# Performance work log

Measured on AMD Instinct MI355X. Metric: run time of the kernel, lower is better.

## Reference

```python
import jax, jax.numpy as jnp
import numpy as np

N_NODES = 50000
N_EDGES = 800000
D_IN = 512
LATENT = [512, 512, 512]
L2_EPS = 1e-12  # torch F.normalize clamp_min


def _gin_layer(x, src, dst, W, b, eps):
    # sum aggregation of neighbor (source) features into destination nodes
    agg = jax.ops.segment_sum(x[src], dst, num_segments=x.shape[0])  # [N, d]
    h = agg + (1.0 + eps) * x
    return jax.nn.relu(h @ W + b)  # Sequential(Linear, ReLU)


def _l2_normalize(x):
    n = jnp.sqrt(jnp.sum(x * x, axis=-1, keepdims=True))
    return x / jnp.maximum(n, L2_EPS)


def setup_inputs() -> dict:
    key = jax.random.key(0)
    ks = jax.random.split(key, 10)
    x = jax.random.normal(ks[0], (N_NODES, D_IN), dtype=jnp.float32)
    edge_index = jax.random.randint(ks[1], (2, N_EDGES), 0, N_NODES, dtype=jnp.int32)
    dims = [D_IN] + LATENT
    inp = {"x": x, "edge_index": edge_index}
    for i in range(3):
        fan_in = dims[i]
        bound = 1.0 / np.sqrt(fan_in)
        inp[f"W{i+1}"] = jax.random.uniform(ks[2 + 2 * i], (dims[i], dims[i + 1]), jnp.float32, -bound, bound)
        inp[f"b{i+1}"] = jax.random.uniform(ks[3 + 2 * i], (dims[i + 1],), jnp.float32, -bound, bound)
        inp[f"eps{i+1}"] = jnp.zeros((), dtype=jnp.float32)  # train_eps=True, init 0
    return inp


def reference(x, edge_index, W1, b1, eps1, W2, b2, eps2, W3, b3, eps3):
    src, dst = edge_index[0], edge_index[1]
    # layers 0..num_layers-2: GINConv -> L2 normalize -> ReLU
    h = _gin_layer(x, src, dst, W1, b1, eps1)
    h = jax.nn.relu(_l2_normalize(h))
    h = _gin_layer(h, src, dst, W2, b2, eps2)
    h = jax.nn.relu(_l2_normalize(h))
    # final layer: raw GINConv output = logits
    logits = _gin_layer(h, src, dst, W3, b3, eps3)
    probs = jax.nn.softmax(logits, axis=-1)
    return (logits, probs)
```

## Files before the change

kernel.cpp:

```cpp
#include <hip/hip_runtime.h>
#include <stdint.h>

#define N_NODES 50000
#define N_EDGES 800000

typedef unsigned int uint32;

__device__ inline float bflo(uint32 u) { return __builtin_bit_cast(float, u << 16); }
__device__ inline float bfhi(uint32 u) { return __builtin_bit_cast(float, u & 0xffff0000u); }
__device__ inline float bf2f(unsigned short h) { return __builtin_bit_cast(float, (uint32)h << 16); }
__device__ inline unsigned short f2bf(float f) {
    uint32 u = __builtin_bit_cast(uint32, f);
    u += 0x7fffu + ((u >> 16) & 1u);
    return (unsigned short)(u >> 16);
}
__device__ inline uint32 pack2(float lo, float hi) {
    return (uint32)f2bf(lo) | ((uint32)f2bf(hi) << 16);
}

__global__ __launch_bounds__(256) void zero_k(int* p, int n) {
    int i = blockIdx.x * 256 + threadIdx.x;
    if (i < n) p[i] = 0;
}

__global__ __launch_bounds__(256) void count_k(const int* __restrict__ ei, int* __restrict__ cnt) {
    int e = blockIdx.x * 256 + threadIdx.x;
    if (e < N_EDGES) atomicAdd(&cnt[ei[N_EDGES + e]], 1);
}

__global__ __launch_bounds__(1024) void scan_k(int* __restrict__ cnt, int* __restrict__ rowptr) {
    __shared__ int sh[1024];
    const int CH = 49;
    int t = threadIdx.x;
    int base = t * CH;
    int s = 0;
    for (int i = 0; i < CH; i++) {
        int idx = base + i;
        if (idx < N_NODES) s += cnt[idx];
    }
    sh[t] = s;
    __syncthreads();
    for (int d = 1; d < 1024; d <<= 1) {
        int v = (t >= d) ? sh[t - d] : 0;
        __syncthreads();
        sh[t] += v;
        __syncthreads();
    }
    int run = sh[t] - s;
    for (int i = 0; i < CH; i++) {
        int idx = base + i;
        if (idx < N_NODES) {
            int v = cnt[idx];
            rowptr[idx] = run;
            cnt[idx] = run;
            run += v;
        }
    }
    if (t == 1023) rowptr[N_NODES] = sh[1023];
}

__global__ __launch_bounds__(256) void fill_k(const int* __restrict__ ei, int* __restrict__ cursor,
                                              int* __restrict__ csr) {
    int e = blockIdx.x * 256 + threadIdx.x;
    if (e < N_EDGES) {
        int d = ei[N_EDGES + e];
        int p = atomicAdd(&cursor[d], 1);
        csr[p] = ei[e];
    }
}

__global__ __launch_bounds__(256) void wprep_k(const float* __restrict__ W,
                                               unsigned short* __restrict__ Whi,
                                               unsigned short* __restrict__ Wlo) {
    int idx = blockIdx.x * 256 + threadIdx.x;
    int k = idx >> 9, n = idx & 511;
    float w = W[idx];
    unsigned short hi = f2bf(w);
    float lo = w - bf2f(hi);
    Whi[n * 512 + k] = hi;
    Wlo[n * 512 + k] = f2bf(lo);
}

__global__ __launch_bounds__(256) void xconv_k(const float* __restrict__ x, uint32* __restrict__ xb) {
    int i = blockIdx.x * 256 + threadIdx.x;
    float2 v = ((const float2*)x)[i];
    xb[i] = pack2(v.x, v.y);
}

__global__ __launch_bounds__(256) void agg_k(const uint32* __restrict__ xin,
                                             const int* __restrict__ rowptr,
                                             const int* __restrict__ csr,
                                             const float* __restrict__ eps,
                                             uint32* __restrict__ hout) {
    int node = blockIdx.x;
    int t = threadIdx.x;
    int beg = rowptr[node], end = rowptr[node + 1];
    const uint32* xc = xin + t;
    float a0 = 0.f, a1 = 0.f;
    int e = beg;
    for (; e + 4 <= end; e += 4) {
        int n0 = csr[e], n1 = csr[e + 1], n2 = csr[e + 2], n3 = csr[e + 3];
        uint32 u0 = xc[n0 * 256], u1 = xc[n1 * 256], u2 = xc[n2 * 256], u3 = xc[n3 * 256];
        a0 += bflo(u0) + bflo(u1) + bflo(u2) + bflo(u3);
        a1 += bfhi(u0) + bfhi(u1) + bfhi(u2) + bfhi(u3);
    }
    for (; e < end; ++e) {
        uint32 u = xc[csr[e] * 256];
        a0 += bflo(u);
        a1 += bfhi(u);
    }
    float ep = 1.0f + eps[0];
    uint32 us = xc[node * 256];
    float h0 = fmaf(ep, bflo(us), a0);
    float h1 = fmaf(ep, bfhi(us), a1);
    hout[node * 256 + t] = pack2(h0, h1);
}

typedef __bf16 bf16x8 __attribute__((ext_vector_type(8)));
typedef float f32x4 __attribute__((ext_vector_type(4)));

template <bool SPLIT, bool F32OUT>
__global__ __launch_bounds__(256) void gemm_k(const unsigned short* __restrict__ A,
                                              const unsigned short* __restrict__ Whi,
                                              const unsigned short* __restrict__ Wlo,
                                              const float* __restrict__ bias,
                                              unsigned short* __restrict__ outB,
                                              float* __restrict__ outF, int M) {
    constexpr int K = 512, N = 512, BK = 32, TM = 128;
    __shared__ unsigned short lds_a[TM * BK];
    __shared__ unsigned short lds_bh[TM * BK];
    __shared__ unsigned short lds_bl[SPLIT ? TM * BK : 16];
    const int t = threadIdx.x;
    const int w = t >> 6, lane = t & 63;
    const int wrow = w >> 1, wcol = w & 1;
    const int m0 = blockIdx.y * TM;
    const int n0 = blockIdx.x * TM;

    int r0 = t >> 2, cc = (t & 3) * 8;
    int r1 = 64 + r0;
    int am0 = m0 + r0; am0 = am0 < M ? am0 : M - 1;
    int am1 = m0 + r1; am1 = am1 < M ? am1 : M - 1;
    const unsigned short* ag0 = A + (size_t)am0 * K + cc;
    const unsigned short* ag1 = A + (size_t)am1 * K + cc;
    const unsigned short* bh0 = Whi + (size_t)(n0 + r0) * K + cc;
    const unsigned short* bh1 = Whi + (size_t)(n0 + r1) * K + cc;
    const unsigned short* bl0 = Wlo + (size_t)(n0 + r0) * K + cc;
    const unsigned short* bl1 = Wlo + (size_t)(n0 + r1) * K + cc;

    f32x4 acc[4][4] = {};
    const int quad = lane >> 4, l15 = lane & 15;
    const int arow = wrow * 64 + l15;
    const int brow = wcol * 64 + l15;

    for (int k0 = 0; k0 < K; k0 += BK) {
        uint4 va0 = *(const uint4*)(ag0 + k0);
        uint4 va1 = *(const uint4*)(ag1 + k0);
        uint4 vh0 = *(const uint4*)(bh0 + k0);
        uint4 vh1 = *(const uint4*)(bh1 + k0);
        uint4 vl0, vl1;
        if (SPLIT) {
            vl0 = *(const uint4*)(bl0 + k0);
            vl1 = *(const uint4*)(bl1 + k0);
        }
        __syncthreads();
        *(uint4*)&lds_a[r0 * BK + cc] = va0;
        *(uint4*)&lds_a[r1 * BK + cc] = va1;
        *(uint4*)&lds_bh[r0 * BK + cc] = vh0;
        *(uint4*)&lds_bh[r1 * BK + cc] = vh1;
        if (SPLIT) {
            *(uint4*)&lds_bl[r0 * BK + cc] = vl0;
            *(uint4*)&lds_bl[r1 * BK + cc] = vl1;
        }
        __syncthreads();
        bf16x8 af[4], bh[4], bl[4];
#pragma unroll
        for (int i = 0; i < 4; i++)
            af[i] = *(const bf16x8*)&lds_a[(arow + i * 16) * BK + quad * 8];
#pragma unroll
        for (int j = 0; j < 4; j++)
            bh[j] = *(const bf16x8*)&lds_bh[(brow + j * 16) * BK + quad * 8];
        if (SPLIT) {
#pragma unroll
            for (int j = 0; j < 4; j++)
                bl[j] = *(const bf16x8*)&lds_bl[(brow + j * 16) * BK + quad * 8];
        }
#pragma unroll
        for (int i = 0; i < 4; i++)
#pragma unroll
            for (int j = 0; j < 4; j++) {
                acc[i][j] = __builtin_amdgcn_mfma_f32_16x16x32_bf16(af[i], bh[j], acc[i][j], 0, 0, 0);
                if (SPLIT)
                    acc[i][j] = __builtin_amdgcn_mfma_f32_16x16x32_bf16(af[i], bl[j], acc[i][j], 0, 0, 0);
            }
    }

#pragma unroll
    for (int j = 0; j < 4; j++) {
        int n = n0 + wcol * 64 + j * 16 + l15;
        float bv = bias[n];
#pragma unroll
        for (int i = 0; i < 4; i++) {
            int mbase = m0 + wrow * 64 + i * 16 + quad * 4;
#pragma unroll
            for (int r = 0; r < 4; r++) {
                int m = mbase + r;
                if (m < M) {
                    float v = fmaxf(acc[i][j][r] + bv, 0.0f);
                    if (F32OUT) outF[(size_t)m * N + n] = v;
                    else        outB[(size_t)m * N + n] = f2bf(v);
                }
            }
        }
    }
}

__global__ __launch_bounds__(256) void l2norm_k(const uint32* __restrict__ z, uint32* __restrict__ out) {
    int node = blockIdx.x * 4 + (threadIdx.x >> 6);
    int lane = threadIdx.x & 63;
    const uint4* zp = (const uint4*)(z + (size_t)node * 256);
    uint4 q = zp[lane];
    float f0 = bflo(q.x), f1 = bfhi(q.x), f2 = bflo(q.y), f3 = bfhi(q.y);
    float f4 = bflo(q.z), f5 = bfhi(q.z), f6 = bflo(q.w), f7 = bfhi(q.w);
    float ss = f0 * f0 + f1 * f1 + f2 * f2 + f3 * f3 + f4 * f4 + f5 * f5 + f6 * f6 + f7 * f7;
#pragma unroll
    for (int off = 32; off > 0; off >>= 1) ss += __shfl_xor(ss, off);
    float inv = 1.0f / fmaxf(sqrtf(ss), 1e-12f);
    uint4 o;
    o.x = pack2(f0 * inv, f1 * inv);
    o.y = pack2(f2 * inv, f3 * inv);
    o.z = pack2(f4 * inv, f5 * inv);
    o.w = pack2(f6 * inv, f7 * inv);
    ((uint4*)(out + (size_t)node * 256))[lane] = o;
}

__global__ __launch_bounds__(256) void softmax_k(const float* __restrict__ logits,
                                                 float* __restrict__ probs) {
    int node = blockIdx.x * 4 + (threadIdx.x >> 6);
    int lane = threadIdx.x & 63;
    const float4* zp = (const float4*)(logits + (size_t)node * 512);
    float4 q0 = zp[lane * 2], q1 = zp[lane * 2 + 1];
    float f[8] = {q0.x, q0.y, q0.z, q0.w, q1.x, q1.y, q1.z, q1.w};
    float m = f[0];
#pragma unroll
    for (int i = 1; i < 8; i++) m = fmaxf(m, f[i]);
#pragma unroll
    for (int off = 32; off > 0; off >>= 1) m = fmaxf(m, __shfl_xor(m, off));
    float e[8], s = 0.f;
#pragma unroll
    for (int i = 0; i < 8; i++) { e[i] = __expf(f[i] - m); s += e[i]; }
#pragma unroll
    for (int off = 32; off > 0; off >>= 1) s += __shfl_xor(s, off);
    float inv = 1.0f / s;
    float4* pp = (float4*)(probs + (size_t)node * 512);
    pp[lane * 2]     = make_float4(e[0] * inv, e[1] * inv, e[2] * inv, e[3] * inv);
    pp[lane * 2 + 1] = make_float4(e[4] * inv, e[5] * inv, e[6] * inv, e[7] * inv);
}

extern "C" void kernel_launch(void* const* d_in, const int* in_sizes, int n_in,
                              void* d_out, int out_size, void* d_ws, size_t ws_size,
                              hipStream_t stream) {
    (void)in_sizes; (void)n_in; (void)out_size; (void)ws_size;
    const float* x = (const float*)d_in[0];
    const int* ei = (const int*)d_in[1];
    const float* W1 = (const float*)d_in[2];
    const float* b1 = (const float*)d_in[3];
    const float* e1 = (const float*)d_in[4];
    const float* W2 = (const float*)d_in[5];
    const float* b2 = (const float*)d_in[6];
    const float* e2 = (const float*)d_in[7];
    const float* W3 = (const float*)d_in[8];
    const float* b3 = (const float*)d_in[9];
    const float* e3 = (const float*)d_in[10];
    float* out = (float*)d_out;
    float* out_logits = out;
    float* out_probs = out + (size_t)N_NODES * 512;

    char* ws = (char*)d_ws;
    int* rowptr = (int*)ws;
    int* cursor = rowptr + 50048;
    int* csr = cursor + 50048;
    unsigned short* Wsp = (unsigned short*)(csr + N_EDGES);
    unsigned short* featA = Wsp + 3 * 524288;
    unsigned short* featB = featA + (size_t)N_NODES * 512;

    zero_k<<<196, 256, 0, stream>>>(cursor, N_NODES);
    count_k<<<(N_EDGES + 255) / 256, 256, 0, stream>>>(ei, cursor);
    scan_k<<<1, 1024, 0, stream>>>(cursor, rowptr);
    fill_k<<<(N_EDGES + 255) / 256, 256, 0, stream>>>(ei, cursor, csr);

    wprep_k<<<1024, 256, 0, stream>>>(W1, Wsp,           Wsp + 262144);
    wprep_k<<<1024, 256, 0, stream>>>(W2, Wsp + 524288,  Wsp + 786432);
    wprep_k<<<1024, 256, 0, stream>>>(W3, Wsp + 1048576, Wsp + 1310720);

    xconv_k<<<50000, 256, 0, stream>>>(x, (uint32*)featB);

    dim3 ggrid(4, (N_NODES + 127) / 128);

    agg_k<<<N_NODES, 256, 0, stream>>>((const uint32*)featB, rowptr, csr, e1, (uint32*)featA);
    gemm_k<false, false><<<ggrid, 256, 0, stream>>>(featA, Wsp, Wsp + 262144, b1, featB, nullptr, N_NODES);
    l2norm_k<<<N_NODES / 4, 256, 0, stream>>>((const uint32*)featB, (uint32*)featB);
    agg_k<<<N_NODES, 256, 0, stream>>>((const uint32*)featB, rowptr, csr, e2, (uint32*)featA);
    gemm_k<false, false><<<ggrid, 256, 0, stream>>>(featA, Wsp + 524288, Wsp + 786432, b2, featB, nullptr, N_NODES);
    l2norm_k<<<N_NODES / 4, 256, 0, stream>>>((const uint32*)featB, (uint32*)featB);
    agg_k<<<N_NODES, 256, 0, stream>>>((const uint32*)featB, rowptr, csr, e3, (uint32*)featA);
    gemm_k<true, true><<<ggrid, 256, 0, stream>>>(featA, Wsp + 1048576, Wsp + 1310720, b3, nullptr, out_logits, N_NODES);
    softmax_k<<<N_NODES / 4, 256, 0, stream>>>(out_logits, out_probs);
}
```

Before: 1.145 ms.

## Split neighbor edges across warps with 16-byte gathers and LDS reduction

The aggregation kernel now assigns each of the four wavefronts a strided subset of a node's edges. Each lane loads a full 16-byte chunk (8 bf16 features) per neighbor, where it previously loaded 4 bytes with all 256 threads walking every edge. Partial sums from wavefronts 1-3 are reduced through shared memory into wavefront 0, which adds the self term and writes the row. This widens memory transactions and spreads edge latency across wavefronts, at the cost of a block barrier, shared-memory traffic, and one idle-heavy final stage.

```diff
diff --git a/kernel.cpp b/kernel.cpp
--- a/kernel.cpp
+++ b/kernel.cpp
@@ -87,33 +87,80 @@
     xb[i] = pack2(v.x, v.y);
 }
 
-__global__ __launch_bounds__(256) void agg_k(const uint32* __restrict__ xin,
+__global__ __launch_bounds__(256) void agg_k(const uint4* __restrict__ xin,
                                              const int* __restrict__ rowptr,
                                              const int* __restrict__ csr,
                                              const float* __restrict__ eps,
-                                             uint32* __restrict__ hout) {
+                                             uint4* __restrict__ hout) {
+    __shared__ float red[8 * 3 * 64];
     int node = blockIdx.x;
-    int t = threadIdx.x;
+    int w = threadIdx.x >> 6, lane = threadIdx.x & 63;
     int beg = rowptr[node], end = rowptr[node + 1];
-    const uint32* xc = xin + t;
-    float a0 = 0.f, a1 = 0.f;
-    int e = beg;
-    for (; e + 4 <= end; e += 4) {
-        int n0 = csr[e], n1 = csr[e + 1], n2 = csr[e + 2], n3 = csr[e + 3];
-        uint32 u0 = xc[n0 * 256], u1 = xc[n1 * 256], u2 = xc[n2 * 256], u3 = xc[n3 * 256];
-        a0 += bflo(u0) + bflo(u1) + bflo(u2) + bflo(u3);
-        a1 += bfhi(u0) + bfhi(u1) + bfhi(u2) + bfhi(u3);
-    }
-    for (; e < end; ++e) {
-        uint32 u = xc[csr[e] * 256];
-        a0 += bflo(u);
-        a1 += bfhi(u);
-    }
-    float ep = 1.0f + eps[0];
-    uint32 us = xc[node * 256];
-    float h0 = fmaf(ep, bflo(us), a0);
-    float h1 = fmaf(ep, bfhi(us), a1);
-    hout[node * 256 + t] = pack2(h0, h1);
+    float a0 = 0.f, a1 = 0.f, a2 = 0.f, a3 = 0.f, a4 = 0.f, a5 = 0.f, a6 = 0.f, a7 = 0.f;
+    int e = beg + w;
+    for (; e + 4 < end; e += 8) {
+        int s0 = csr[e], s1 = csr[e + 4];
+        uint4 q0 = xin[(size_t)s0 * 64 + lane];
+        uint4 q1 = xin[(size_t)s1 * 64 + lane];
+        a0 += bflo(q0.x) + bflo(q1.x);
+        a1 += bfhi(q0.x) + bfhi(q1.x);
+        a2 += bflo(q0.y) + bflo(q1.y);
+        a3 += bfhi(q0.y) + bfhi(q1.y);
+        a4 += bflo(q0.z) + bflo(q1.z);
+        a5 += bfhi(q0.z) + bfhi(q1.z);
+        a6 += bflo(q0.w) + bflo(q1.w);
+        a7 += bfhi(q0.w) + bfhi(q1.w);
+    }
+    if (e < end) {
+        int s0 = csr[e];
+        uint4 q0 = xin[(size_t)s0 * 64 + lane];
+        a0 += bflo(q0.x); a1 += bfhi(q0.x);
+        a2 += bflo(q0.y); a3 += bfhi(q0.y);
+        a4 += bflo(q0.z); a5 += bfhi(q0.z);
+        a6 += bflo(q0.w); a7 += bfhi(q0.w);
+    }
+    if (w > 0) {
+        int base = (w - 1) * 64 + lane;
+        red[0 * 192 + base] = a0;
+        red[1 * 192 + base] = a1;
+        red[2 * 192 + base] = a2;
+        red[3 * 192 + base] = a3;
+        red[4 * 192 + base] = a4;
+        red[5 * 192 + base] = a5;
+        red[6 * 192 + base] = a6;
+        red[7 * 192 + base] = a7;
+    }
+    __syncthreads();
+    if (w == 0) {
+        uint4 qs = xin[(size_t)node * 64 + lane];
+        float ep = 1.0f + eps[0];
+#pragma unroll
+        for (int p = 0; p < 3; p++) {
+            int base = p * 64 + lane;
+            a0 += red[0 * 192 + base];
+            a1 += red[1 * 192 + base];
+            a2 += red[2 * 192 + base];
+            a3 += red[3 * 192 + base];
+            a4 += red[4 * 192 + base];
+            a5 += red[5 * 192 + base];
+            a6 += red[6 * 192 + base];
+            a7 += red[7 * 192 + base];
+        }
+        a0 = fmaf(ep, bflo(qs.x), a0);
+        a1 = fmaf(ep, bfhi(qs.x), a1);
+        a2 = fmaf(ep, bflo(qs.y), a2);
+        a3 = fmaf(ep, bfhi(qs.y), a3);
+        a4 = fmaf(ep, bflo(qs.z), a4);
+        a5 = fmaf(ep, bfhi(qs.z), a5);
+        a6 = fmaf(ep, bflo(qs.w), a6);
+        a7 = fmaf(ep, bfhi(qs.w), a7);
+        uint4 o;
+        o.x = pack2(a0, a1);
+        o.y = pack2(a2, a3);
+        o.z = pack2(a4, a5);
+        o.w = pack2(a6, a7);
+        hout[(size_t)node * 64 + lane] = o;
+    }
 }
 
 typedef __bf16 bf16x8 __attribute__((ext_vector_type(8)));
@@ -296,13 +343,13 @@
 
     dim3 ggrid(4, (N_NODES + 127) / 128);
 
-    agg_k<<<N_NODES, 256, 0, stream>>>((const uint32*)featB, rowptr, csr, e1, (uint32*)featA);
+    agg_k<<<N_NODES, 256, 0, stream>>>((const uint4*)featB, rowptr, csr, e1, (uint4*)featA);
     gemm_k<false, false><<<ggrid, 256, 0, stream>>>(featA, Wsp, Wsp + 262144, b1, featB, nullptr, N_NODES);
     l2norm_k<<<N_NODES / 4, 256, 0, stream>>>((const uint32*)featB, (uint32*)featB);
-    agg_k<<<N_NODES, 256, 0, stream>>>((const uint32*)featB, rowptr, csr, e2, (uint32*)featA);
+    agg_k<<<N_NODES, 256, 0, stream>>>((const uint4*)featB, rowptr, csr, e2, (uint4*)featA);
     gemm_k<false, false><<<ggrid, 256, 0, stream>>>(featA, Wsp + 524288, Wsp + 786432, b2, featB, nullptr, N_NODES);
     l2norm_k<<<N_NODES / 4, 256, 0, stream>>>((const uint32*)featB, (uint32*)featB);
-    agg_k<<<N_NODES, 256, 0, stream>>>((const uint32*)featB, rowptr, csr, e3, (uint32*)featA);
+    agg_k<<<N_NODES, 256, 0, stream>>>((const uint4*)featB, rowptr, csr, e3, (uint4*)featA);
     gemm_k<true, true><<<ggrid, 256, 0, stream>>>(featA, Wsp + 1048576, Wsp + 1310720, b3, nullptr, out_logits, N_NODES);
     softmax_k<<<N_NODES / 4, 256, 0, stream>>>(out_logits, out_probs);
 }
```

Result: no change. 1.148 ms (+0.3%).

## Fold L2 normalization into aggregation, vectorize gather, async LDS loads in GEMM

Applied to the files above, without the earlier changes.

The separate normalize-and-rewrite pass becomes a kernel that only computes per-node inverse norms. Aggregation applies those norms as per-neighbor weights, which removes one full feature-matrix write. Aggregation now uses one wavefront per node with 16-byte loads per lane instead of 4-byte loads per thread. The GEMM stages tiles via global_load_lds async copies instead of going through registers. Rounding now differs slightly, because normalized features are no longer rounded to bf16 before aggregation.

```diff
diff --git a/kernel.cpp b/kernel.cpp
--- a/kernel.cpp
+++ b/kernel.cpp
@@ -87,37 +87,79 @@
     xb[i] = pack2(v.x, v.y);
 }
 
-__global__ __launch_bounds__(256) void agg_k(const uint32* __restrict__ xin,
+__global__ __launch_bounds__(256) void norm_k(const uint4* __restrict__ z, float* __restrict__ invn) {
+    int node = blockIdx.x * 4 + (threadIdx.x >> 6);
+    int lane = threadIdx.x & 63;
+    uint4 q = z[(size_t)node * 64 + lane];
+    float f0 = bflo(q.x), f1 = bfhi(q.x), f2 = bflo(q.y), f3 = bfhi(q.y);
+    float f4 = bflo(q.z), f5 = bfhi(q.z), f6 = bflo(q.w), f7 = bfhi(q.w);
+    float ss = f0 * f0 + f1 * f1 + f2 * f2 + f3 * f3 + f4 * f4 + f5 * f5 + f6 * f6 + f7 * f7;
+#pragma unroll
+    for (int off = 32; off > 0; off >>= 1) ss += __shfl_xor(ss, off);
+    if (lane == 0) invn[node] = 1.0f / fmaxf(sqrtf(ss), 1e-12f);
+}
+
+template <bool SCALED>
+__global__ __launch_bounds__(256) void agg_k(const uint4* __restrict__ xin,
                                              const int* __restrict__ rowptr,
                                              const int* __restrict__ csr,
                                              const float* __restrict__ eps,
-                                             uint32* __restrict__ hout) {
-    int node = blockIdx.x;
-    int t = threadIdx.x;
+                                             const float* __restrict__ invn,
+                                             uint4* __restrict__ hout) {
+    int node = blockIdx.x * 4 + (threadIdx.x >> 6);
+    int lane = threadIdx.x & 63;
     int beg = rowptr[node], end = rowptr[node + 1];
-    const uint32* xc = xin + t;
-    float a0 = 0.f, a1 = 0.f;
+    float a0 = 0.f, a1 = 0.f, a2 = 0.f, a3 = 0.f, a4 = 0.f, a5 = 0.f, a6 = 0.f, a7 = 0.f;
     int e = beg;
     for (; e + 4 <= end; e += 4) {
-        int n0 = csr[e], n1 = csr[e + 1], n2 = csr[e + 2], n3 = csr[e + 3];
-        uint32 u0 = xc[n0 * 256], u1 = xc[n1 * 256], u2 = xc[n2 * 256], u3 = xc[n3 * 256];
-        a0 += bflo(u0) + bflo(u1) + bflo(u2) + bflo(u3);
-        a1 += bfhi(u0) + bfhi(u1) + bfhi(u2) + bfhi(u3);
+        int s0 = csr[e], s1 = csr[e + 1], s2 = csr[e + 2], s3 = csr[e + 3];
+        uint4 q0 = xin[(size_t)s0 * 64 + lane];
+        uint4 q1 = xin[(size_t)s1 * 64 + lane];
+        uint4 q2 = xin[(size_t)s2 * 64 + lane];
+        uint4 q3 = xin[(size_t)s3 * 64 + lane];
+        float w0 = SCALED ? invn[s0] : 1.0f;
+        float w1 = SCALED ? invn[s1] : 1.0f;
+        float w2 = SCALED ? invn[s2] : 1.0f;
+        float w3 = SCALED ? invn[s3] : 1.0f;
+        a0 = fmaf(w0, bflo(q0.x), fmaf(w1, bflo(q1.x), fmaf(w2, bflo(q2.x), fmaf(w3, bflo(q3.x), a0))));
+        a1 = fmaf(w0, bfhi(q0.x), fmaf(w1, bfhi(q1.x), fmaf(w2, bfhi(q2.x), fmaf(w3, bfhi(q3.x), a1))));
+        a2 = fmaf(w0, bflo(q0.y), fmaf(w1, bflo(q1.y), fmaf(w2, bflo(q2.y), fmaf(w3, bflo(q3.y), a2))));
+        a3 = fmaf(w0, bfhi(q0.y), fmaf(w1, bfhi(q1.y), fmaf(w2, bfhi(q2.y), fmaf(w3, bfhi(q3.y), a3))));
+        a4 = fmaf(w0, bflo(q0.z), fmaf(w1, bflo(q1.z), fmaf(w2, bflo(q2.z), fmaf(w3, bflo(q3.z), a4))));
+        a5 = fmaf(w0, bfhi(q0.z), fmaf(w1, bfhi(q1.z), fmaf(w2, bfhi(q2.z), fmaf(w3, bfhi(q3.z), a5))));
+        a6 = fmaf(w0, bflo(q0.w), fmaf(w1, bflo(q1.w), fmaf(w2, bflo(q2.w), fmaf(w3, bflo(q3.w), a6))));
+        a7 = fmaf(w0, bfhi(q0.w), fmaf(w1, bfhi(q1.w), fmaf(w2, bfhi(q2.w), fmaf(w3, bfhi(q3.w), a7))));
     }
     for (; e < end; ++e) {
-        uint32 u = xc[csr[e] * 256];
-        a0 += bflo(u);
-        a1 += bfhi(u);
-    }
-    float ep = 1.0f + eps[0];
-    uint32 us = xc[node * 256];
-    float h0 = fmaf(ep, bflo(us), a0);
-    float h1 = fmaf(ep, bfhi(us), a1);
-    hout[node * 256 + t] = pack2(h0, h1);
+        int s0 = csr[e];
+        uint4 q0 = xin[(size_t)s0 * 64 + lane];
+        float w0 = SCALED ? invn[s0] : 1.0f;
+        a0 = fmaf(w0, bflo(q0.x), a0); a1 = fmaf(w0, bfhi(q0.x), a1);
+        a2 = fmaf(w0, bflo(q0.y), a2); a3 = fmaf(w0, bfhi(q0.y), a3);
+        a4 = fmaf(w0, bflo(q0.z), a4); a5 = fmaf(w0, bfhi(q0.z), a5);
+        a6 = fmaf(w0, bflo(q0.w), a6); a7 = fmaf(w0, bfhi(q0.w), a7);
+    }
+    uint4 qs = xin[(size_t)node * 64 + lane];
+    float ws = (1.0f + eps[0]) * (SCALED ? invn[node] : 1.0f);
+    a0 = fmaf(ws, bflo(qs.x), a0); a1 = fmaf(ws, bfhi(qs.x), a1);
+    a2 = fmaf(ws, bflo(qs.y), a2); a3 = fmaf(ws, bfhi(qs.y), a3);
+    a4 = fmaf(ws, bflo(qs.z), a4); a5 = fmaf(ws, bfhi(qs.z), a5);
+    a6 = fmaf(ws, bflo(qs.w), a6); a7 = fmaf(ws, bfhi(qs.w), a7);
+    uint4 o;
+    o.x = pack2(a0, a1);
+    o.y = pack2(a2, a3);
+    o.z = pack2(a4, a5);
+    o.w = pack2(a6, a7);
+    hout[(size_t)node * 64 + lane] = o;
 }
 
 typedef __bf16 bf16x8 __attribute__((ext_vector_type(8)));
 typedef float f32x4 __attribute__((ext_vector_type(4)));
+
+__device__ inline void async16(const void* g, void* l) {
+    __builtin_amdgcn_global_load_lds((const __attribute__((address_space(1))) void*)g,
+                                     (__attribute__((address_space(3))) void*)l, 16, 0, 0);
+}
 
 template <bool SPLIT, bool F32OUT>
 __global__ __launch_bounds__(256) void gemm_k(const unsigned short* __restrict__ A,
@@ -136,7 +178,7 @@
     const int m0 = blockIdx.y * TM;
     const int n0 = blockIdx.x * TM;
 
-    int r0 = t >> 2, cc = (t & 3) * 8;
+    int r0 = w * 16 + (lane >> 2), cc = (lane & 3) * 8;
     int r1 = 64 + r0;
     int am0 = m0 + r0; am0 = am0 < M ? am0 : M - 1;
     int am1 = m0 + r1; am1 = am1 < M ? am1 : M - 1;
@@ -146,6 +188,12 @@
     const unsigned short* bh1 = Whi + (size_t)(n0 + r1) * K + cc;
     const unsigned short* bl0 = Wlo + (size_t)(n0 + r0) * K + cc;
     const unsigned short* bl1 = Wlo + (size_t)(n0 + r1) * K + cc;
+    unsigned short* la0 = lds_a + w * 512;
+    unsigned short* la1 = lds_a + 2048 + w * 512;
+    unsigned short* lh0 = lds_bh + w * 512;
+    unsigned short* lh1 = lds_bh + 2048 + w * 512;
+    unsigned short* ll0 = lds_bl + w * 512;
+    unsigned short* ll1 = lds_bl + 2048 + w * 512;
 
     f32x4 acc[4][4] = {};
     const int quad = lane >> 4, l15 = lane & 15;
@@ -153,23 +201,14 @@
     const int brow = wcol * 64 + l15;
 
     for (int k0 = 0; k0 < K; k0 += BK) {
-        uint4 va0 = *(const uint4*)(ag0 + k0);
-        uint4 va1 = *(const uint4*)(ag1 + k0);
-        uint4 vh0 = *(const uint4*)(bh0 + k0);
-        uint4 vh1 = *(const uint4*)(bh1 + k0);
-        uint4 vl0, vl1;
+        __syncthreads();
+        async16(ag0 + k0, la0);
+        async16(ag1 + k0, la1);
+        async16(bh0 + k0, lh0);
+        async16(bh1 + k0, lh1);
         if (SPLIT) {
-            vl0 = *(const uint4*)(bl0 + k0);
-            vl1 = *(const uint4*)(bl1 + k0);
-        }
-        __syncthreads();
-        *(uint4*)&lds_a[r0 * BK + cc] = va0;
-        *(uint4*)&lds_a[r1 * BK + cc] = va1;
-        *(uint4*)&lds_bh[r0 * BK + cc] = vh0;
-        *(uint4*)&lds_bh[r1 * BK + cc] = vh1;
-        if (SPLIT) {
-            *(uint4*)&lds_bl[r0 * BK + cc] = vl0;
-            *(uint4*)&lds_bl[r1 * BK + cc] = vl1;
+            async16(bl0 + k0, ll0);
+            async16(bl1 + k0, ll1);
         }
         __syncthreads();
         bf16x8 af[4], bh[4], bl[4];
@@ -212,25 +251,6 @@
             }
         }
     }
-}
-
-__global__ __launch_bounds__(256) void l2norm_k(const uint32* __restrict__ z, uint32* __restrict__ out) {
-    int node = blockIdx.x * 4 + (threadIdx.x >> 6);
-    int lane = threadIdx.x & 63;
-    const uint4* zp = (const uint4*)(z + (size_t)node * 256);
-    uint4 q = zp[lane];
-    float f0 = bflo(q.x), f1 = bfhi(q.x), f2 = bflo(q.y), f3 = bfhi(q.y);
-    float f4 = bflo(q.z), f5 = bfhi(q.z), f6 = bflo(q.w), f7 = bfhi(q.w);
-    float ss = f0 * f0 + f1 * f1 + f2 * f2 + f3 * f3 + f4 * f4 + f5 * f5 + f6 * f6 + f7 * f7;
-#pragma unroll
-    for (int off = 32; off > 0; off >>= 1) ss += __shfl_xor(ss, off);
-    float inv = 1.0f / fmaxf(sqrtf(ss), 1e-12f);
-    uint4 o;
-    o.x = pack2(f0 * inv, f1 * inv);
-    o.y = pack2(f2 * inv, f3 * inv);
-    o.z = pack2(f4 * inv, f5 * inv);
-    o.w = pack2(f6 * inv, f7 * inv);
-    ((uint4*)(out + (size_t)node * 256))[lane] = o;
 }
 
 __global__ __launch_bounds__(256) void softmax_k(const float* __restrict__ logits,
@@ -279,7 +299,8 @@
     int* rowptr = (int*)ws;
     int* cursor = rowptr + 50048;
     int* csr = cursor + 50048;
-    unsigned short* Wsp = (unsigned short*)(csr + N_EDGES);
+    float* invn = (float*)(csr + N_EDGES);
+    unsigned short* Wsp = (unsigned short*)(invn + 50048);
     unsigned short* featA = Wsp + 3 * 524288;
     unsigned short* featB = featA + (size_t)N_NODES * 512;
 
@@ -296,13 +317,13 @@
 
     dim3 ggrid(4, (N_NODES + 127) / 128);
 
-    agg_k<<<N_NODES, 256, 0, stream>>>((const uint32*)featB, rowptr, csr, e1, (uint32*)featA);
+    agg_k<false><<<12500, 256, 0, stream>>>((const uint4*)featB, rowptr, csr, e1, nullptr, (uint4*)featA);
     gemm_k<false, false><<<ggrid, 256, 0, stream>>>(featA, Wsp, Wsp + 262144, b1, featB, nullptr, N_NODES);
-    l2norm_k<<<N_NODES / 4, 256, 0, stream>>>((const uint32*)featB, (uint32*)featB);
-    agg_k<<<N_NODES, 256, 0, stream>>>((const uint32*)featB, rowptr, csr, e2, (uint32*)featA);
+    norm_k<<<12500, 256, 0, stream>>>((const uint4*)featB, invn);
+    agg_k<true><<<12500, 256, 0, stream>>>((const uint4*)featB, rowptr, csr, e2, invn, (uint4*)featA);
     gemm_k<false, false><<<ggrid, 256, 0, stream>>>(featA, Wsp + 524288, Wsp + 786432, b2, featB, nullptr, N_NODES);
-    l2norm_k<<<N_NODES / 4, 256, 0, stream>>>((const uint32*)featB, (uint32*)featB);
-    agg_k<<<N_NODES, 256, 0, stream>>>((const uint32*)featB, rowptr, csr, e3, (uint32*)featA);
+    norm_k<<<12500, 256, 0, stream>>>((const uint4*)featB, invn);
+    agg_k<true><<<12500, 256, 0, stream>>>((const uint4*)featB, rowptr, csr, e3, invn, (uint4*)featA);
     gemm_k<true, true><<<ggrid, 256, 0, stream>>>(featA, Wsp + 1048576, Wsp + 1310720, b3, nullptr, out_logits, N_NODES);
     softmax_k<<<N_NODES / 4, 256, 0, stream>>>(out_logits, out_probs);
 }
```

Result: no change. 1.146 ms (+0.1%).
